# Kernel tuning notes

Measured on AMD Instinct MI355X. Metric: run time of the kernel, lower is better.

Reference implementation:

```python
import jax, jax.numpy as jnp
import numpy as np

KERNEL = 25  # moving_avg
E_LAYERS = 2
D_LAYERS = 1
N_HEADS = 8
D_MODEL = 512
ENC_IN = 7
C_OUT = 7


def series_decomp(x, k=KERNEL):
    # x: [B, L, D]; AvgPool1d(kernel=k, stride=1, padding=k//2, count_include_pad=True)
    pad = k // 2
    xp = jnp.pad(x, ((0, 0), (pad, pad), (0, 0)))
    cs = jnp.pad(jnp.cumsum(xp, axis=1), ((0, 0), (1, 0), (0, 0)))
    trend = (cs[:, k:, :] - cs[:, :-k, :]) / k  # [B, L, D]
    return x - trend, trend


def autocorrelation(q, k, v, n_heads=N_HEADS):
    B, L, E = q.shape
    S = k.shape[1]
    d = E // n_heads
    qh = q.reshape(B, L, n_heads, d).transpose(0, 2, 1, 3)  # [B,H,L,d]
    kh = k.reshape(B, S, n_heads, d).transpose(0, 2, 1, 3)  # [B,H,S,d]
    vh = v.reshape(B, S, n_heads, d).transpose(0, 2, 3, 1)  # [B,H,d,S]
    # NOTE: faithful to source, FFT is over the head dim d; irfft pads freq bins to n=L
    qf = jnp.fft.rfft(qh, axis=-1)
    kf = jnp.fft.rfft(kh, axis=-1)
    corr = jnp.fft.irfft(qf * jnp.conj(kf), n=L, axis=-1)  # [B,H,L,L]
    mean_v = jnp.mean(corr, axis=1, keepdims=True)
    w = jax.nn.softmax(corr - mean_v, axis=-1)
    w = jnp.swapaxes(w, -1, -2)                      # [B,H,L,L]
    V = jnp.matmul(w, jnp.swapaxes(vh, -1, -2))      # [B,H,L,d]
    V = jnp.swapaxes(V, -1, -2)                      # [B,H,d,L]
    # torch: V.permute(0,2,1,3).reshape(B, L, -1) (row-major reinterpretation)
    out = V.transpose(0, 2, 1, 3).reshape(B, L, -1)  # [B,L,E]
    return out


def setup_inputs() -> dict:
    key = jax.random.key(0)
    ks = jax.random.split(key, 10)
    B, L = 8, 1024
    inp = {
        "x_enc": jax.random.normal(ks[0], (B, L, ENC_IN), jnp.float32),
        "x_mark_enc": jax.random.normal(ks[1], (B, L, 4), jnp.float32),
        "x_dec": jax.random.normal(ks[2], (B, L, ENC_IN), jnp.float32),
        "x_mark_dec": jax.random.normal(ks[3], (B, L, 4), jnp.float32),
        "enc_w": jax.random.normal(ks[4], (ENC_IN, D_MODEL), jnp.float32) * 0.1,
        "enc_b": jnp.zeros((D_MODEL,), jnp.float32),
        "dec_w": jax.random.normal(ks[5], (ENC_IN, D_MODEL), jnp.float32) * 0.1,
        "dec_b": jnp.zeros((D_MODEL,), jnp.float32),
        "proj_w": jax.random.normal(ks[6], (D_MODEL, C_OUT), jnp.float32) * 0.05,
        "proj_b": jnp.zeros((C_OUT,), jnp.float32),
    }
    return inp


def reference(x_enc, x_mark_enc, x_dec, x_mark_dec, enc_w, enc_b, dec_w, dec_b, proj_w, proj_b):
    enc_out = x_enc @ enc_w + enc_b      # [B,L,D]
    dec_emb = x_dec @ dec_w + dec_b      # [B,L,D]
    enc_seasonal, enc_trend = series_decomp(enc_out)
    for _ in range(E_LAYERS):
        enc_seasonal = autocorrelation(enc_seasonal, enc_seasonal, enc_seasonal)
    seasonal, trend = series_decomp(dec_emb)
    for _ in range(D_LAYERS):
        seasonal = autocorrelation(seasonal, enc_seasonal, enc_seasonal)
        trend = trend + enc_trend
    dec_out = seasonal + trend
    return dec_out @ proj_w + proj_b     # [B,L,c_out]
```

## Files before the change

### kernel.cpp

```cpp
#include <hip/hip_runtime.h>
#include <hip/hip_bf16.h>

#define BB 8
#define LL 1024
#define DD 512
#define NH 8
#define DH 64
#define CO 7
#define GK 64
#define MM 8192

typedef __hip_bfloat16 bf16;
typedef __attribute__((ext_vector_type(8))) short short8;
typedef __attribute__((ext_vector_type(4))) float floatx4;
typedef __attribute__((ext_vector_type(4))) unsigned short ushort4v;

__device__ __forceinline__ float b2f(bf16 v){ return __bfloat162float(v); }
__device__ __forceinline__ bf16 f2b(float v){ return __float2bfloat16(v); }
__device__ __forceinline__ unsigned short f2bu(float v){
    bf16 h = f2b(v); return *(unsigned short*)&h;
}
__device__ __forceinline__ float bu2f(unsigned short u){
    union{unsigned i; float f;} x; x.i = ((unsigned)u)<<16; return x.f;
}

__global__ void sniff_kernel(const unsigned* __restrict__ x, int* __restrict__ flag){
    unsigned u = x[threadIdx.x];
    int e = (u >> 23) & 0xff;
    int sane = (e >= 32 && e <= 200) ? 1 : 0;
    unsigned long long m = __ballot(sane);
    if(threadIdx.x == 0) *flag = (__popcll(m) >= 32) ? 1 : 0;
}

__global__ __launch_bounds__(256) void ma7_kernel(const void* __restrict__ xv,
                                                  const int* __restrict__ flag,
                                                  float* __restrict__ xs,
                                                  float* __restrict__ xm){
    int idx = blockIdx.x*256 + threadIdx.x;
    if(idx >= BB*LL*7) return;
    bool f32 = (*flag != 0);
    int i = idx % 7;
    int row = idx / 7;
    int l = row & (LL-1);
    int b = row >> 10;
    int lo = l-12; if(lo<0) lo=0;
    int hi = l+12; if(hi>LL-1) hi=LL-1;
    float s = 0.f, xc;
    if(f32){
        const float* x = (const float*)xv + ((size_t)b*LL)*7 + i;
        for(int m=lo;m<=hi;m++) s += x[(size_t)m*7];
        xc = x[(size_t)l*7];
    }else{
        const bf16* x = (const bf16*)xv + ((size_t)b*LL)*7 + i;
        for(int m=lo;m<=hi;m++) s += b2f(x[(size_t)m*7]);
        xc = b2f(x[(size_t)l*7]);
    }
    float ma = s*(1.f/25.f);
    xm[idx] = ma;
    xs[idx] = xc - ma;
}

__global__ __launch_bounds__(256) void embed2_kernel(const float* __restrict__ xs,
                                                     const float* __restrict__ xm,
                                                     const void* __restrict__ wv,
                                                     const void* __restrict__ bv,
                                                     const int* __restrict__ flag,
                                                     bf16* __restrict__ seas,
                                                     bf16* __restrict__ trend,
                                                     int accumulate){
    bool f32 = (*flag != 0);
    int row = blockIdx.x >> 1;
    int d = ((blockIdx.x & 1) << 8) + threadIdx.x;
    int idx = row*DD + d;
    int l = row & (LL-1);
    int lo = l-12; if(lo<0) lo=0;
    int hi = l+12; if(hi>LL-1) hi=LL-1;
    float cf = (float)(hi-lo+1) * (1.f/25.f);
    float wcol[7], bias;
    if(f32){
        const float* w = (const float*)wv;
        #pragma unroll
        for(int i=0;i<7;i++) wcol[i] = w[i*DD + d];
        bias = ((const float*)bv)[d];
    }else{
        const bf16* w = (const bf16*)wv;
        #pragma unroll
        for(int i=0;i<7;i++) wcol[i] = b2f(w[i*DD + d]);
        bias = b2f(((const bf16*)bv)[d]);
    }
    float sa = 0.f, ta = 0.f;
    #pragma unroll
    for(int i=0;i<7;i++){
        sa += xs[row*7+i]*wcol[i];
        ta += xm[row*7+i]*wcol[i];
    }
    seas[idx] = f2b(sa + bias*(1.f-cf));
    float t = ta + bias*cf;
    if(accumulate) t += b2f(trend[idx]);
    trend[idx] = f2b(t);
}

__global__ __launch_bounds__(64) void trig_init(bf16* __restrict__ Tg){
    int t = blockIdx.x, k = threadIdx.x;
    int f = (k >> 1) + 1;
    int ph = (f*t) & 1023;
    float s, c;
    __sincosf((float)ph * (6.28318530717958647692f/1024.f), &s, &c);
    Tg[(size_t)t*GK + k] = f2b((k & 1) ? s : c);
}

__global__ __launch_bounds__(64) void tw_init(bf16* __restrict__ Tw){
    int j = threadIdx.x, k = blockIdx.x;
    int f = (k >> 1) + 1;
    int ph = (f*j) & 63;
    float s, c;
    __sincosf((float)ph * (6.28318530717958647692f/64.f), &s, &c);
    Tw[(size_t)k*64 + j] = f2b((k & 1) ? -s : c);
}

__global__ __launch_bounds__(512) void pwt_init(const void* __restrict__ pwv,
                                                const int* __restrict__ flag,
                                                float* __restrict__ pwT){
    bool f32 = (*flag != 0);
    int c = blockIdx.x, d = threadIdx.x;
    float v = f32 ? ((const float*)pwv)[(size_t)d*CO + c]
                  : b2f(((const bf16*)pwv)[(size_t)d*CO + c]);
    pwT[(size_t)c*DD + d] = v;
}

__global__ __launch_bounds__(256) void dft2(const bf16* __restrict__ qg,
                                            const bf16* __restrict__ kg,
                                            const bf16* __restrict__ Tw,
                                            bf16* __restrict__ Ab,
                                            int same_qk){
    __shared__ __align__(16) unsigned short Tl[64][68];
    int tid = threadIdx.x, wv = tid >> 6, lane = tid & 63;
    int qd = lane >> 4, n = lane & 15;
    int m0 = blockIdx.x*64 + wv*16;
    const short* qp = (const short*)qg;
    const short* kp = (const short*)kg;
    const short* tw = (const short*)Tw;
    short8 aq0 = *(const short8*)&qp[(size_t)(m0+n)*64 + qd*8];
    short8 aq1 = *(const short8*)&qp[(size_t)(m0+n)*64 + 32 + qd*8];
    short8 bw[4][2];
    #pragma unroll
    for(int nt=0;nt<4;nt++){
        bw[nt][0] = *(const short8*)&tw[(size_t)(nt*16+n)*64 + qd*8];
        bw[nt][1] = *(const short8*)&tw[(size_t)(nt*16+n)*64 + 32 + qd*8];
    }
    floatx4 dq[4], dk[4];
    #pragma unroll
    for(int nt=0;nt<4;nt++){
        floatx4 a = {};
        a = __builtin_amdgcn_mfma_f32_16x16x32_bf16(aq0, bw[nt][0], a, 0,0,0);
        a = __builtin_amdgcn_mfma_f32_16x16x32_bf16(aq1, bw[nt][1], a, 0,0,0);
        dq[nt] = a;
    }
    if(same_qk){
        #pragma unroll
        for(int nt=0;nt<4;nt++) dk[nt] = dq[nt];
    }else{
        short8 ak0 = *(const short8*)&kp[(size_t)(m0+n)*64 + qd*8];
        short8 ak1 = *(const short8*)&kp[(size_t)(m0+n)*64 + 32 + qd*8];
        #pragma unroll
        for(int nt=0;nt<4;nt++){
            floatx4 a = {};
            a = __builtin_amdgcn_mfma_f32_16x16x32_bf16(ak0, bw[nt][0], a, 0,0,0);
            a = __builtin_amdgcn_mfma_f32_16x16x32_bf16(ak1, bw[nt][1], a, 0,0,0);
            dk[nt] = a;
        }
    }
    #pragma unroll
    for(int nt=0;nt<4;nt++){
        float o[4];
        #pragma unroll
        for(int r=0;r<4;r++){
            float a  = dq[nt][r], pa = __shfl_xor(a, 1);
            float c  = dk[nt][r], pc = __shfl_xor(c, 1);
            o[r] = (n & 1) ? (pa*c - a*pc) : (a*c + pa*pc);
        }
        float s = o[0]+o[1]+o[2]+o[3];
        s += __shfl_xor(s, 16);
        float mean = s*0.125f;
        #pragma unroll
        for(int r=0;r<4;r++)
            Tl[wv*16 + qd*4 + r][nt*16 + n] = f2bu((o[r]-mean)*(1.f/512.f));
    }
    __syncthreads();
    int h2 = tid >> 5, lloc = (tid & 31) >> 2, c4 = tid & 3;
    int lr = lloc*8 + h2;
    int bI = blockIdx.x >> 7;
    int l  = (blockIdx.x & 127)*8 + lloc;
    union { ushort4v h[4]; short8 s[2]; } w;
    const unsigned short* src = &Tl[lr][c4*16];
    w.h[0] = *(const ushort4v*)(src);
    w.h[1] = *(const ushort4v*)(src+4);
    w.h[2] = *(const ushort4v*)(src+8);
    w.h[3] = *(const ushort4v*)(src+12);
    short* dp = (short*)Ab + ((size_t)bI*MM + (size_t)h2*LL + l)*GK + c4*16;
    *(short8*)dp       = w.s[0];
    *(short8*)(dp + 8) = w.s[1];
}

__global__ __launch_bounds__(256) void rowstats3(const bf16* __restrict__ Ab,
                                                 const bf16* __restrict__ Tg,
                                                 float* __restrict__ rs){
    __shared__ float red[4][64];
    int tid = threadIdx.x, wv = tid >> 6, lane = tid & 63;
    int q = lane >> 4, n = lane & 15;
    int m0 = blockIdx.x*64, bloc = blockIdx.y;
    const short* Abase = (const short*)(Ab + ((size_t)bloc*MM)*GK);
    const short* Tb = (const short*)Tg;
    short8 af[4][2];
    #pragma unroll
    for(int mg=0;mg<4;mg++){
        af[mg][0] = *(const short8*)&Abase[(size_t)(m0+mg*16+n)*GK + q*8];
        af[mg][1] = *(const short8*)&Abase[(size_t)(m0+mg*16+n)*GK + 32 + q*8];
    }
    float s[4][4] = {};
    #pragma unroll
    for(int nt=0;nt<16;nt++){
        int t = wv*256 + nt*16 + n;
        short8 b0 = *(const short8*)&Tb[(size_t)t*GK + q*8];
        short8 b1 = *(const short8*)&Tb[(size_t)t*GK + 32 + q*8];
        #pragma unroll
        for(int mg=0;mg<4;mg++){
            floatx4 d = {};
            d = __builtin_amdgcn_mfma_f32_16x16x32_bf16(af[mg][0], b0, d, 0,0,0);
            d = __builtin_amdgcn_mfma_f32_16x16x32_bf16(af[mg][1], b1, d, 0,0,0);
            #pragma unroll
            for(int r=0;r<4;r++) s[mg][r] += __expf(d[r]);
        }
    }
    #pragma unroll
    for(int o=1;o<16;o<<=1)
        #pragma unroll
        for(int mg=0;mg<4;mg++)
            #pragma unroll
            for(int r=0;r<4;r++) s[mg][r] += __shfl_xor(s[mg][r], o, 64);
    if(n == 0){
        #pragma unroll
        for(int mg=0;mg<4;mg++)
            #pragma unroll
            for(int r=0;r<4;r++) red[wv][mg*16 + q*4 + r] = s[mg][r];
    }
    __syncthreads();
    if(tid < 64)
        rs[(size_t)bloc*MM + m0 + tid] =
            -__logf(red[0][tid]+red[1][tid]+red[2][tid]+red[3][tid]);
}

__global__ __launch_bounds__(256) void vt_kernel(const bf16* __restrict__ v,
                                                 bf16* __restrict__ vt){
    __shared__ unsigned short T2[64][68];
    int jc = blockIdx.x, h = blockIdx.y, b = blockIdx.z;
    int tid = threadIdx.x;
    const unsigned short* src = (const unsigned short*)v + ((size_t)b*LL)*DD + (size_t)h*DH;
    int cq = tid & 15, jq = tid >> 4;
    #pragma unroll
    for(int jr=0;jr<4;jr++){
        int jl = jq*4 + jr;
        ushort4v vv = *(const ushort4v*)&src[(size_t)(jc*64 + jl)*DD + cq*4];
        T2[cq*4+0][jl] = vv.x;
        T2[cq*4+1][jl] = vv.y;
        T2[cq*4+2][jl] = vv.z;
        T2[cq*4+3][jl] = vv.w;
    }
    __syncthreads();
    int j4 = tid & 15, ct = tid >> 4;
    unsigned short* dstb = (unsigned short*)vt + ((size_t)(b*NH + h))*64*LL + (size_t)jc*64;
    #pragma unroll
    for(int cc=0;cc<4;cc++){
        int c = cc*16 + ct;
        *(ushort4v*)&dstb[(size_t)c*LL + j4*4] = *(const ushort4v*)&T2[c][j4*4];
    }
}

__global__ __launch_bounds__(256, 2) void fused_pv(const bf16* __restrict__ Ab,
                                                   const bf16* __restrict__ Tg,
                                                   const float* __restrict__ rs,
                                                   const bf16* __restrict__ vt,
                                                   bf16* __restrict__ dst){
    __shared__ __align__(16) unsigned short AbS[2][64][68];
    __shared__ __align__(16) unsigned short VsS[2][64][68];
    __shared__ __align__(16) unsigned short Pl[128][68];
    __shared__ float stS[LL];
    int tid = threadIdx.x, wv = tid >> 6, lane = tid & 63;
    int q = lane >> 4, n = lane & 15;
    int id = blockIdx.x;
    int xcd = id & 7, p = id >> 3;
    int pair = xcd*8 + (p & 7);
    int i0 = (p >> 3) * 128;
    int h = pair & 7, bloc = pair >> 3;
    const short* Abase = (const short*)(Ab + ((size_t)bloc*MM + (size_t)h*LL)*GK);
    const short* Tb = (const short*)Tg;
    const float* rsb = rs + (size_t)bloc*MM + (size_t)h*LL;
    const short* vtb = (const short*)(vt + (size_t)pair*64*LL);

    *(floatx4*)&stS[tid*4] = *(const floatx4*)&rsb[tid*4];

    short8 tgf[2][2];
    #pragma unroll
    for(int t2=0;t2<2;t2++){
        tgf[t2][0] = *(const short8*)&Tb[(size_t)(i0+wv*32+t2*16+n)*GK + q*8];
        tgf[t2][1] = *(const short8*)&Tb[(size_t)(i0+wv*32+t2*16+n)*GK + 32 + q*8];
    }

    int srow = tid >> 2, sc = (tid & 3) * 16;
    const short* agp = &Abase[(size_t)srow*GK + sc];
    const short* vgp = &vtb[(size_t)srow*LL + sc];

    union S8 { short8 s; ushort4v h[2]; };

    {
        S8 a0,a1,v0,v1;
        a0.s = *(const short8*)agp;       a1.s = *(const short8*)(agp+8);
        v0.s = *(const short8*)vgp;       v1.s = *(const short8*)(vgp+8);
        *(ushort4v*)&AbS[0][srow][sc]    = a0.h[0];
        *(ushort4v*)&AbS[0][srow][sc+4]  = a0.h[1];
        *(ushort4v*)&AbS[0][srow][sc+8]  = a1.h[0];
        *(ushort4v*)&AbS[0][srow][sc+12] = a1.h[1];
        *(ushort4v*)&VsS[0][srow][sc]    = v0.h[0];
        *(ushort4v*)&VsS[0][srow][sc+4]  = v0.h[1];
        *(ushort4v*)&VsS[0][srow][sc+8]  = v1.h[0];
        *(ushort4v*)&VsS[0][srow][sc+12] = v1.h[1];
    }
    __syncthreads();

    floatx4 acc[4][2] = {};
    int cur = 0;
    for(int it=0; it<16; ++it){
        int j0 = it*64;
        S8 na0,na1,nv0,nv1;
        if(it < 15){
            na0.s = *(const short8*)(agp + (size_t)(j0+64)*GK);
            na1.s = *(const short8*)(agp + (size_t)(j0+64)*GK + 8);
            nv0.s = *(const short8*)(vgp + (j0+64));
            nv1.s = *(const short8*)(vgp + (j0+64) + 8);
        }
        #pragma unroll
        for(int tj=0;tj<4;tj++){
            S8 a0,a1;
            const unsigned short* ar = &AbS[cur][tj*16+n][0];
            a0.h[0] = *(const ushort4v*)&ar[q*8];
            a0.h[1] = *(const ushort4v*)&ar[q*8+4];
            a1.h[0] = *(const ushort4v*)&ar[32+q*8];
            a1.h[1] = *(const ushort4v*)&ar[32+q*8+4];
            floatx4 c0 = *(const floatx4*)&stS[j0 + tj*16 + q*4];
            #pragma unroll
            for(int t2=0;t2<2;t2++){
                floatx4 d = c0;
                d = __builtin_amdgcn_mfma_f32_16x16x32_bf16(a0.s, tgf[t2][0], d, 0,0,0);
                d = __builtin_amdgcn_mfma_f32_16x16x32_bf16(a1.s, tgf[t2][1], d, 0,0,0);
                ushort4v pk;
                pk.x = f2bu(__expf(d[0]));
                pk.y = f2bu(__expf(d[1]));
                pk.z = f2bu(__expf(d[2]));
                pk.w = f2bu(__expf(d[3]));
                *(ushort4v*)&Pl[wv*32 + t2*16 + n][tj*16 + q*4] = pk;
            }
        }
        #pragma unroll
        for(int kc=0;kc<2;kc++){
            S8 va[4];
            #pragma unroll
            for(int cs=0;cs<4;cs++){
                const unsigned short* vp = &VsS[cur][cs*16+n][kc*32+q*8];
                va[cs].h[0] = *(const ushort4v*)vp;
                va[cs].h[1] = *(const ushort4v*)(vp+4);
            }
            #pragma unroll
            for(int t2=0;t2<2;t2++){
                S8 pf;
                const unsigned short* pp = &Pl[wv*32 + t2*16 + n][kc*32 + q*8];
                pf.h[0] = *(const ushort4v*)pp;
                pf.h[1] = *(const ushort4v*)(pp+4);
                #pragma unroll
                for(int cs=0;cs<4;cs++)
                    acc[cs][t2] = __builtin_amdgcn_mfma_f32_16x16x32_bf16(va[cs].s, pf.s, acc[cs][t2], 0,0,0);
            }
        }
        if(it < 15){
            int nb = cur ^ 1;
            *(ushort4v*)&AbS[nb][srow][sc]    = na0.h[0];
            *(ushort4v*)&AbS[nb][srow][sc+4]  = na0.h[1];
            *(ushort4v*)&AbS[nb][srow][sc+8]  = na1.h[0];
            *(ushort4v*)&AbS[nb][srow][sc+12] = na1.h[1];
            *(ushort4v*)&VsS[nb][srow][sc]    = nv0.h[0];
            *(ushort4v*)&VsS[nb][srow][sc+4]  = nv0.h[1];
            *(ushort4v*)&VsS[nb][srow][sc+8]  = nv1.h[0];
            *(ushort4v*)&VsS[nb][srow][sc+12] = nv1.h[1];
        }
        __syncthreads();
        cur ^= 1;
    }
    bf16* db = dst + (size_t)bloc*LL*DD;
    #pragma unroll
    for(int t2=0;t2<2;t2++){
        int i = i0 + wv*32 + t2*16 + n;
        #pragma unroll
        for(int cs=0;cs<4;cs++){
            #pragma unroll
            for(int r=0;r<4;r++){
                int c = cs*16 + q*4 + r;
                db[(size_t)c*MM + h*LL + i] = f2b(acc[cs][t2][r]);
            }
        }
    }
}

__global__ __launch_bounds__(64) void final_kernel(const bf16* __restrict__ s,
                                                   const bf16* __restrict__ t,
                                                   const float* __restrict__ pwT,
                                                   const void* __restrict__ pbv,
                                                   const int* __restrict__ flag,
                                                   void* __restrict__ outv){
    bool f32 = (*flag != 0);
    int row = blockIdx.x;
    int lane = threadIdx.x;
    const short* sr = (const short*)s + (size_t)row*DD;
    const short* tr = (const short*)t + (size_t)row*DD;
    int j0 = lane*8;
    union { short8 v; unsigned short u[8]; } s8, t8;
    s8.v = *(const short8*)&sr[j0];
    t8.v = *(const short8*)&tr[j0];
    float dv[8];
    #pragma unroll
    for(int jj=0;jj<8;jj++) dv[jj] = bu2f(s8.u[jj]) + bu2f(t8.u[jj]);
    float acc[CO];
    #pragma unroll
    for(int c=0;c<CO;c++){
        floatx4 w0 = *(const floatx4*)&pwT[(size_t)c*DD + j0];
        floatx4 w1 = *(const floatx4*)&pwT[(size_t)c*DD + j0 + 4];
        acc[c] = dv[0]*w0[0] + dv[1]*w0[1] + dv[2]*w0[2] + dv[3]*w0[3]
               + dv[4]*w1[0] + dv[5]*w1[1] + dv[6]*w1[2] + dv[7]*w1[3];
    }
    #pragma unroll
    for(int c=0;c<CO;c++){
        float vsum = acc[c];
        for(int off=32;off;off>>=1) vsum += __shfl_down(vsum,off,64);
        if(lane==0){
            float bias = f32 ? ((const float*)pbv)[c] : b2f(((const bf16*)pbv)[c]);
            float o = vsum + bias;
            if(f32) ((float*)outv)[(size_t)row*CO + c] = o;
            else    ((bf16*)outv)[(size_t)row*CO + c] = f2b(o);
        }
    }
}

extern "C" void kernel_launch(void* const* d_in, const int* in_sizes, int n_in,
                              void* d_out, int out_size, void* d_ws, size_t ws_size,
                              hipStream_t stream){
    const void* x_enc  = d_in[0];
    const void* x_dec  = d_in[2];
    const void* enc_w  = d_in[4];
    const void* enc_b  = d_in[5];
    const void* dec_w  = d_in[6];
    const void* dec_b  = d_in[7];
    const void* proj_w = d_in[8];
    const void* proj_b = d_in[9];

    int*  flag = (int*)d_ws;
    const size_t NE = (size_t)BB*LL*DD;
    bf16* A  = (bf16*)((char*)d_ws + 1024);
    bf16* Bf = A  + NE;
    bf16* C  = Bf + NE;
    bf16* T  = C  + NE;
    bf16* Tg = T  + NE;
    bf16* Tw = Tg + (size_t)LL*GK;
    float* xs = (float*)(Tw + 64*64);
    float* xm = xs + (size_t)BB*LL*7;
    bf16* Ab  = (bf16*)(xm + (size_t)BB*LL*7);
    float* rs = (float*)(Ab + (size_t)BB*MM*GK);
    bf16* Vt  = (bf16*)(rs + (size_t)BB*MM);
    float* pwT = (float*)(Vt + (size_t)BB*NH*64*LL);

    sniff_kernel<<<1,64,0,stream>>>((const unsigned*)x_enc, flag);
    trig_init<<<LL,64,0,stream>>>(Tg);
    tw_init<<<64,64,0,stream>>>(Tw);
    pwt_init<<<CO,512,0,stream>>>(proj_w, flag, pwT);

    auto autocorr = [&](const bf16* q, const bf16* kv, bf16* dst){
        vt_kernel<<<dim3(16, NH, BB), 256, 0, stream>>>(kv, Vt);
        dft2<<<1024, 256, 0, stream>>>(q, kv, Tw, Ab, (q==kv) ? 1 : 0);
        rowstats3<<<dim3(128, BB), 256, 0, stream>>>(Ab, Tg, rs);
        fused_pv<<<512, 256, 0, stream>>>(Ab, Tg, rs, Vt, dst);
    };

    const int MA_GRID = (BB*LL*7 + 255)/256;
    ma7_kernel<<<MA_GRID,256,0,stream>>>(x_enc, flag, xs, xm);
    embed2_kernel<<<16384,256,0,stream>>>(xs, xm, enc_w, enc_b, flag, A, T, 0);
    autocorr(A, A, Bf);
    autocorr(Bf, Bf, A);

    ma7_kernel<<<MA_GRID,256,0,stream>>>(x_dec, flag, xs, xm);
    embed2_kernel<<<16384,256,0,stream>>>(xs, xm, dec_w, dec_b, flag, Bf, T, 1);
    autocorr(Bf, A, C);

    final_kernel<<<BB*LL,64,0,stream>>>(C, T, pwT, proj_b, flag, d_out);
}
```

Baseline: 315.7 us.

## Merge init kernels, fuse moving average into embedding, widen LDS accesses

The three table-init kernels become one prep kernel. The moving-average kernel is folded into the embedding kernel, which computes the 7 channel averages in shared memory per row, so two launches and the xs/xm round trip go away. In fused_pv the LDS row pitch changes from 68 to 72 so that 16-byte short8 loads and stores replace paired 8-byte accesses. The new pitch may alter the LDS bank-conflict pattern, and each embedding block now has only 7 threads doing a serial 25-tap window sum before the rest of the block can proceed.

New measurement: 347.7 us. 1.1x slower.

```diff
diff --git a/kernel.cpp b/kernel.cpp
--- a/kernel.cpp
+++ b/kernel.cpp
@@ -9,6 +9,7 @@
 #define CO 7
 #define GK 64
 #define MM 8192
+#define PLS 72
 
 typedef __hip_bfloat16 bf16;
 typedef __attribute__((ext_vector_type(8))) short short8;
@@ -32,49 +33,67 @@
     if(threadIdx.x == 0) *flag = (__popcll(m) >= 32) ? 1 : 0;
 }
 
-__global__ __launch_bounds__(256) void ma7_kernel(const void* __restrict__ xv,
-                                                  const int* __restrict__ flag,
-                                                  float* __restrict__ xs,
-                                                  float* __restrict__ xm){
-    int idx = blockIdx.x*256 + threadIdx.x;
-    if(idx >= BB*LL*7) return;
+__global__ __launch_bounds__(512) void prep_kernel(bf16* __restrict__ Tg,
+                                                   bf16* __restrict__ Tw,
+                                                   const void* __restrict__ pwv,
+                                                   const int* __restrict__ flag,
+                                                   float* __restrict__ pwT){
+    int blk = blockIdx.x, tid = threadIdx.x;
+    if(blk < 128){
+        int t = blk*8 + (tid >> 6), k = tid & 63;
+        int f = (k >> 1) + 1;
+        int ph = (f*t) & 1023;
+        float s, c;
+        __sincosf((float)ph * (6.28318530717958647692f/1024.f), &s, &c);
+        Tg[(size_t)t*GK + k] = f2b((k & 1) ? s : c);
+    } else if(blk < 136){
+        int idx = (blk-128)*512 + tid;
+        int k = idx >> 6, j = idx & 63;
+        int f = (k >> 1) + 1;
+        int ph = (f*j) & 63;
+        float s, c;
+        __sincosf((float)ph * (6.28318530717958647692f/64.f), &s, &c);
+        Tw[(size_t)k*64 + j] = f2b((k & 1) ? -s : c);
+    } else {
+        int c = blk - 136, d = tid;
+        bool f32 = (*flag != 0);
+        float v = f32 ? ((const float*)pwv)[(size_t)d*CO + c]
+                      : b2f(((const bf16*)pwv)[(size_t)d*CO + c]);
+        pwT[(size_t)c*DD + d] = v;
+    }
+}
+
+__global__ __launch_bounds__(512) void embed2f(const void* __restrict__ xv,
+                                               const void* __restrict__ wv,
+                                               const void* __restrict__ bv,
+                                               const int* __restrict__ flag,
+                                               bf16* __restrict__ seas,
+                                               bf16* __restrict__ trend,
+                                               int accumulate){
+    __shared__ float sxs[8], sxm[8];
     bool f32 = (*flag != 0);
-    int i = idx % 7;
-    int row = idx / 7;
-    int l = row & (LL-1);
-    int b = row >> 10;
+    int row = blockIdx.x;
+    int l = row & (LL-1), b = row >> 10;
+    int lane = threadIdx.x;
     int lo = l-12; if(lo<0) lo=0;
     int hi = l+12; if(hi>LL-1) hi=LL-1;
-    float s = 0.f, xc;
-    if(f32){
-        const float* x = (const float*)xv + ((size_t)b*LL)*7 + i;
-        for(int m=lo;m<=hi;m++) s += x[(size_t)m*7];
-        xc = x[(size_t)l*7];
-    }else{
-        const bf16* x = (const bf16*)xv + ((size_t)b*LL)*7 + i;
-        for(int m=lo;m<=hi;m++) s += b2f(x[(size_t)m*7]);
-        xc = b2f(x[(size_t)l*7]);
-    }
-    float ma = s*(1.f/25.f);
-    xm[idx] = ma;
-    xs[idx] = xc - ma;
-}
-
-__global__ __launch_bounds__(256) void embed2_kernel(const float* __restrict__ xs,
-                                                     const float* __restrict__ xm,
-                                                     const void* __restrict__ wv,
-                                                     const void* __restrict__ bv,
-                                                     const int* __restrict__ flag,
-                                                     bf16* __restrict__ seas,
-                                                     bf16* __restrict__ trend,
-                                                     int accumulate){
-    bool f32 = (*flag != 0);
-    int row = blockIdx.x >> 1;
-    int d = ((blockIdx.x & 1) << 8) + threadIdx.x;
-    int idx = row*DD + d;
-    int l = row & (LL-1);
-    int lo = l-12; if(lo<0) lo=0;
-    int hi = l+12; if(hi>LL-1) hi=LL-1;
+    if(lane < 7){
+        float s = 0.f, xc;
+        if(f32){
+            const float* x = (const float*)xv + ((size_t)b*LL)*7 + lane;
+            for(int m=lo;m<=hi;m++) s += x[(size_t)m*7];
+            xc = x[(size_t)l*7];
+        }else{
+            const bf16* x = (const bf16*)xv + ((size_t)b*LL)*7 + lane;
+            for(int m=lo;m<=hi;m++) s += b2f(x[(size_t)m*7]);
+            xc = b2f(x[(size_t)l*7]);
+        }
+        float ma = s*(1.f/25.f);
+        sxm[lane] = ma;
+        sxs[lane] = xc - ma;
+    }
+    __syncthreads();
+    int d = lane;
     float cf = (float)(hi-lo+1) * (1.f/25.f);
     float wcol[7], bias;
     if(f32){
@@ -91,41 +110,14 @@
     float sa = 0.f, ta = 0.f;
     #pragma unroll
     for(int i=0;i<7;i++){
-        sa += xs[row*7+i]*wcol[i];
-        ta += xm[row*7+i]*wcol[i];
-    }
+        sa += sxs[i]*wcol[i];
+        ta += sxm[i]*wcol[i];
+    }
+    int idx = row*DD + d;
     seas[idx] = f2b(sa + bias*(1.f-cf));
     float t = ta + bias*cf;
     if(accumulate) t += b2f(trend[idx]);
     trend[idx] = f2b(t);
-}
-
-__global__ __launch_bounds__(64) void trig_init(bf16* __restrict__ Tg){
-    int t = blockIdx.x, k = threadIdx.x;
-    int f = (k >> 1) + 1;
-    int ph = (f*t) & 1023;
-    float s, c;
-    __sincosf((float)ph * (6.28318530717958647692f/1024.f), &s, &c);
-    Tg[(size_t)t*GK + k] = f2b((k & 1) ? s : c);
-}
-
-__global__ __launch_bounds__(64) void tw_init(bf16* __restrict__ Tw){
-    int j = threadIdx.x, k = blockIdx.x;
-    int f = (k >> 1) + 1;
-    int ph = (f*j) & 63;
-    float s, c;
-    __sincosf((float)ph * (6.28318530717958647692f/64.f), &s, &c);
-    Tw[(size_t)k*64 + j] = f2b((k & 1) ? -s : c);
-}
-
-__global__ __launch_bounds__(512) void pwt_init(const void* __restrict__ pwv,
-                                                const int* __restrict__ flag,
-                                                float* __restrict__ pwT){
-    bool f32 = (*flag != 0);
-    int c = blockIdx.x, d = threadIdx.x;
-    float v = f32 ? ((const float*)pwv)[(size_t)d*CO + c]
-                  : b2f(((const bf16*)pwv)[(size_t)d*CO + c]);
-    pwT[(size_t)c*DD + d] = v;
 }
 
 __global__ __launch_bounds__(256) void dft2(const bf16* __restrict__ qg,
@@ -281,9 +273,9 @@
                                                    const float* __restrict__ rs,
                                                    const bf16* __restrict__ vt,
                                                    bf16* __restrict__ dst){
-    __shared__ __align__(16) unsigned short AbS[2][64][68];
-    __shared__ __align__(16) unsigned short VsS[2][64][68];
-    __shared__ __align__(16) unsigned short Pl[128][68];
+    __shared__ __align__(16) unsigned short AbS[2][64][PLS];
+    __shared__ __align__(16) unsigned short VsS[2][64][PLS];
+    __shared__ __align__(16) unsigned short Pl[128][PLS];
     __shared__ float stS[LL];
     int tid = threadIdx.x, wv = tid >> 6, lane = tid & 63;
     int q = lane >> 4, n = lane & 15;
@@ -310,20 +302,15 @@
     const short* agp = &Abase[(size_t)srow*GK + sc];
     const short* vgp = &vtb[(size_t)srow*LL + sc];
 
-    union S8 { short8 s; ushort4v h[2]; };
-
     {
-        S8 a0,a1,v0,v1;
-        a0.s = *(const short8*)agp;       a1.s = *(const short8*)(agp+8);
-        v0.s = *(const short8*)vgp;       v1.s = *(const short8*)(vgp+8);
-        *(ushort4v*)&AbS[0][srow][sc]    = a0.h[0];
-        *(ushort4v*)&AbS[0][srow][sc+4]  = a0.h[1];
-        *(ushort4v*)&AbS[0][srow][sc+8]  = a1.h[0];
-        *(ushort4v*)&AbS[0][srow][sc+12] = a1.h[1];
-        *(ushort4v*)&VsS[0][srow][sc]    = v0.h[0];
-        *(ushort4v*)&VsS[0][srow][sc+4]  = v0.h[1];
-        *(ushort4v*)&VsS[0][srow][sc+8]  = v1.h[0];
-        *(ushort4v*)&VsS[0][srow][sc+12] = v1.h[1];
+        short8 a0 = *(const short8*)agp;
+        short8 a1 = *(const short8*)(agp+8);
+        short8 v0 = *(const short8*)vgp;
+        short8 v1 = *(const short8*)(vgp+8);
+        *(short8*)&AbS[0][srow][sc]   = a0;
+        *(short8*)&AbS[0][srow][sc+8] = a1;
+        *(short8*)&VsS[0][srow][sc]   = v0;
+        *(short8*)&VsS[0][srow][sc+8] = v1;
     }
     __syncthreads();
 
@@ -331,27 +318,23 @@
     int cur = 0;
     for(int it=0; it<16; ++it){
         int j0 = it*64;
-        S8 na0,na1,nv0,nv1;
+        short8 na0, na1, nv0, nv1;
         if(it < 15){
-            na0.s = *(const short8*)(agp + (size_t)(j0+64)*GK);
-            na1.s = *(const short8*)(agp + (size_t)(j0+64)*GK + 8);
-            nv0.s = *(const short8*)(vgp + (j0+64));
-            nv1.s = *(const short8*)(vgp + (j0+64) + 8);
+            na0 = *(const short8*)(agp + (size_t)(j0+64)*GK);
+            na1 = *(const short8*)(agp + (size_t)(j0+64)*GK + 8);
+            nv0 = *(const short8*)(vgp + (j0+64));
+            nv1 = *(const short8*)(vgp + (j0+64) + 8);
         }
         #pragma unroll
         for(int tj=0;tj<4;tj++){
-            S8 a0,a1;
-            const unsigned short* ar = &AbS[cur][tj*16+n][0];
-            a0.h[0] = *(const ushort4v*)&ar[q*8];
-            a0.h[1] = *(const ushort4v*)&ar[q*8+4];
-            a1.h[0] = *(const ushort4v*)&ar[32+q*8];
-            a1.h[1] = *(const ushort4v*)&ar[32+q*8+4];
+            short8 a0 = *(const short8*)&AbS[cur][tj*16+n][q*8];
+            short8 a1 = *(const short8*)&AbS[cur][tj*16+n][32+q*8];
             floatx4 c0 = *(const floatx4*)&stS[j0 + tj*16 + q*4];
             #pragma unroll
             for(int t2=0;t2<2;t2++){
                 floatx4 d = c0;
-                d = __builtin_amdgcn_mfma_f32_16x16x32_bf16(a0.s, tgf[t2][0], d, 0,0,0);
-                d = __builtin_amdgcn_mfma_f32_16x16x32_bf16(a1.s, tgf[t2][1], d, 0,0,0);
+                d = __builtin_amdgcn_mfma_f32_16x16x32_bf16(a0, tgf[t2][0], d, 0,0,0);
+                d = __builtin_amdgcn_mfma_f32_16x16x32_bf16(a1, tgf[t2][1], d, 0,0,0);
                 ushort4v pk;
                 pk.x = f2bu(__expf(d[0]));
                 pk.y = f2bu(__expf(d[1]));
@@ -362,34 +345,24 @@
         }
         #pragma unroll
         for(int kc=0;kc<2;kc++){
-            S8 va[4];
-            #pragma unroll
-            for(int cs=0;cs<4;cs++){
-                const unsigned short* vp = &VsS[cur][cs*16+n][kc*32+q*8];
-                va[cs].h[0] = *(const ushort4v*)vp;
-                va[cs].h[1] = *(const ushort4v*)(vp+4);
-            }
+            short8 va[4];
+            #pragma unroll
+            for(int cs=0;cs<4;cs++)
+                va[cs] = *(const short8*)&VsS[cur][cs*16+n][kc*32+q*8];
             #pragma unroll
             for(int t2=0;t2<2;t2++){
-                S8 pf;
-                const unsigned short* pp = &Pl[wv*32 + t2*16 + n][kc*32 + q*8];
-                pf.h[0] = *(const ushort4v*)pp;
-                pf.h[1] = *(const ushort4v*)(pp+4);
+                short8 pf = *(const short8*)&Pl[wv*32 + t2*16 + n][kc*32 + q*8];
                 #pragma unroll
                 for(int cs=0;cs<4;cs++)
-                    acc[cs][t2] = __builtin_amdgcn_mfma_f32_16x16x32_bf16(va[cs].s, pf.s, acc[cs][t2], 0,0,0);
+                    acc[cs][t2] = __builtin_amdgcn_mfma_f32_16x16x32_bf16(va[cs], pf, acc[cs][t2], 0,0,0);
             }
         }
         if(it < 15){
             int nb = cur ^ 1;
-            *(ushort4v*)&AbS[nb][srow][sc]    = na0.h[0];
-            *(ushort4v*)&AbS[nb][srow][sc+4]  = na0.h[1];
-            *(ushort4v*)&AbS[nb][srow][sc+8]  = na1.h[0];
-            *(ushort4v*)&AbS[nb][srow][sc+12] = na1.h[1];
-            *(ushort4v*)&VsS[nb][srow][sc]    = nv0.h[0];
-            *(ushort4v*)&VsS[nb][srow][sc+4]  = nv0.h[1];
-            *(ushort4v*)&VsS[nb][srow][sc+8]  = nv1.h[0];
-            *(ushort4v*)&VsS[nb][srow][sc+12] = nv1.h[1];
+            *(short8*)&AbS[nb][srow][sc]   = na0;
+            *(short8*)&AbS[nb][srow][sc+8] = na1;
+            *(short8*)&VsS[nb][srow][sc]   = nv0;
+            *(short8*)&VsS[nb][srow][sc+8] = nv1;
         }
         __syncthreads();
         cur ^= 1;
@@ -476,9 +449,7 @@
     float* pwT = (float*)(Vt + (size_t)BB*NH*64*LL);
 
     sniff_kernel<<<1,64,0,stream>>>((const unsigned*)x_enc, flag);
-    trig_init<<<LL,64,0,stream>>>(Tg);
-    tw_init<<<64,64,0,stream>>>(Tw);
-    pwt_init<<<CO,512,0,stream>>>(proj_w, flag, pwT);
+    prep_kernel<<<143,512,0,stream>>>(Tg, Tw, proj_w, flag, pwT);
 
     auto autocorr = [&](const bf16* q, const bf16* kv, bf16* dst){
         vt_kernel<<<dim3(16, NH, BB), 256, 0, stream>>>(kv, Vt);
@@ -487,14 +458,11 @@
         fused_pv<<<512, 256, 0, stream>>>(Ab, Tg, rs, Vt, dst);
     };
 
-    const int MA_GRID = (BB*LL*7 + 255)/256;
-    ma7_kernel<<<MA_GRID,256,0,stream>>>(x_enc, flag, xs, xm);
-    embed2_kernel<<<16384,256,0,stream>>>(xs, xm, enc_w, enc_b, flag, A, T, 0);
+    embed2f<<<BB*LL,512,0,stream>>>(x_enc, enc_w, enc_b, flag, A, T, 0);
     autocorr(A, A, Bf);
     autocorr(Bf, Bf, A);
 
-    ma7_kernel<<<MA_GRID,256,0,stream>>>(x_dec, flag, xs, xm);
-    embed2_kernel<<<16384,256,0,stream>>>(xs, xm, dec_w, dec_b, flag, Bf, T, 1);
+    embed2f<<<BB*LL,512,0,stream>>>(x_dec, dec_w, dec_b, flag, Bf, T, 1);
     autocorr(Bf, A, C);
 
     final_kernel<<<BB*LL,64,0,stream>>>(C, T, pwT, proj_b, flag, d_out);
```
